# Performance work log

Measured on AMD Instinct MI355X. Metric: run time of the kernel, lower is better.

The kernel has to match this reference:

```python
import jax, jax.numpy as jnp
import numpy as np

N, E = 100000, 800000
H, C = 4, 32
HC = H * C


def setup_inputs() -> dict:
    key = jax.random.key(0)
    ks = jax.random.split(key, 32)

    def lin(k, fi, fo):
        return jax.random.normal(k, (fi, fo), jnp.float32) / np.sqrt(fi)

    inp = {
        "x": jax.random.normal(ks[0], (N, 2), jnp.float32),
        "edge_index": jax.random.randint(ks[1], (2, E), 0, N, jnp.int64),
        "edge_attr": jax.random.normal(ks[2], (E, 1), jnp.float32),
        # layer 0 (in=2)
        "Wq0": lin(ks[3], 2, HC), "bq0": jnp.zeros((HC,), jnp.float32),
        "Wk0": lin(ks[4], 2, HC), "bk0": jnp.zeros((HC,), jnp.float32),
        "Wv0": lin(ks[5], 2, HC), "bv0": jnp.zeros((HC,), jnp.float32),
        "We0": lin(ks[6], 1, HC),
        "Ws0": lin(ks[7], 2, HC), "bs0": jnp.zeros((HC,), jnp.float32),
        # layer 1 (in=HC)
        "Wq1": lin(ks[8], HC, HC), "bq1": jnp.zeros((HC,), jnp.float32),
        "Wk1": lin(ks[9], HC, HC), "bk1": jnp.zeros((HC,), jnp.float32),
        "Wv1": lin(ks[10], HC, HC), "bv1": jnp.zeros((HC,), jnp.float32),
        "We1": lin(ks[11], 1, HC),
        "Ws1": lin(ks[12], HC, HC), "bs1": jnp.zeros((HC,), jnp.float32),
        # classifier
        "Wc1": lin(ks[13], HC, 128), "bc1": jnp.zeros((128,), jnp.float32),
        "Wc2": lin(ks[14], 128, 64), "bc2": jnp.zeros((64,), jnp.float32),
        "Wc3": lin(ks[15], 64, 1), "bc3": jnp.zeros((1,), jnp.float32),
    }
    return inp


def _tconv(x, src, dst, edge_attr, Wq, bq, Wk, bk, Wv, bv, We, Ws, bs):
    # PyG TransformerConv (concat=True, root_weight=True, beta=False)
    n = x.shape[0]
    q = (x @ Wq + bq).reshape(n, H, C)
    k = (x @ Wk + bk).reshape(n, H, C)
    v = (x @ Wv + bv).reshape(n, H, C)
    e = (edge_attr @ We).reshape(-1, H, C)            # [E,H,C]
    k_j = k[src] + e
    v_j = v[src] + e
    alpha = jnp.einsum("ehc,ehc->eh", q[dst], k_j) / np.sqrt(C)  # [E,H]
    m = jax.ops.segment_max(alpha, dst, num_segments=n)          # [n,H]
    m = jnp.where(jnp.isfinite(m), m, 0.0)            # nodes with no in-edges
    ex = jnp.exp(alpha - m[dst])
    denom = jax.ops.segment_sum(ex, dst, num_segments=n)
    w = ex / (denom[dst] + 1e-16)                      # per-edge softmax weight
    out = jax.ops.segment_sum(v_j * w[:, :, None], dst, num_segments=n)
    return out.reshape(n, HC) + x @ Ws + bs


def reference(x, edge_index, edge_attr,
              Wq0, bq0, Wk0, bk0, Wv0, bv0, We0, Ws0, bs0,
              Wq1, bq1, Wk1, bk1, Wv1, bv1, We1, Ws1, bs1,
              Wc1, bc1, Wc2, bc2, Wc3, bc3):
    src, dst = edge_index[0], edge_index[1]
    h = jax.nn.relu(_tconv(x, src, dst, edge_attr, Wq0, bq0, Wk0, bk0, Wv0, bv0, We0, Ws0, bs0))
    h = jax.nn.relu(_tconv(h, src, dst, edge_attr, Wq1, bq1, Wk1, bk1, Wv1, bv1, We1, Ws1, bs1))
    # classifier (dropout inactive in eval)
    h = jax.nn.relu(h @ Wc1 + bc1)
    h = jax.nn.relu(h @ Wc2 + bc2)
    return h @ Wc3 + bc3
```

## Files before the change

### kernel.cpp

```cpp
#include <hip/hip_runtime.h>
#include <hip/hip_bf16.h>
#include <cstdio>
#include <cstdint>


typedef short s16x8 __attribute__((ext_vector_type(8)));
typedef float f32x4 __attribute__((ext_vector_type(4)));

static inline int cdiv(int a, int b) { return (a + b - 1) / b; }

#define EXP2F(x) __builtin_amdgcn_exp2f(x)
#define LOG2E 1.4426950408889634f
#define RSC 0.17677669529663687f

__device__ __forceinline__ float bflo(unsigned u) {
    union { unsigned i; float f; } x; x.i = u << 16; return x.f;
}
__device__ __forceinline__ float bfhi(unsigned u) {
    union { unsigned i; float f; } x; x.i = u & 0xffff0000u; return x.f;
}
__device__ __forceinline__ unsigned short f2b(float f) {
    __hip_bfloat16 h = __float2bfloat16(f);
    return *reinterpret_cast<unsigned short*>(&h);
}
__device__ __forceinline__ unsigned packbf(float lo, float hi) {
    return (unsigned)f2b(lo) | ((unsigned)f2b(hi) << 16);
}


__global__ __launch_bounds__(256) void hist_kernel(const int* __restrict__ dst, int E,
                                                   int* __restrict__ counts) {
    int e = blockIdx.x * 256 + threadIdx.x;
    if (e < E) atomicAdd(&counts[dst[e]], 1);
}

__global__ __launch_bounds__(256) void scan_sums(const int* __restrict__ counts, int n,
                                                 int* __restrict__ bsums) {
    __shared__ int red[256];
    int base = blockIdx.x * 2048 + threadIdx.x * 8;
    int s = 0;
#pragma unroll
    for (int j = 0; j < 8; ++j) {
        int i = base + j;
        if (i < n) s += counts[i];
    }
    red[threadIdx.x] = s;
    __syncthreads();
    for (int off = 128; off > 0; off >>= 1) {
        if (threadIdx.x < off) red[threadIdx.x] += red[threadIdx.x + off];
        __syncthreads();
    }
    if (threadIdx.x == 0) bsums[blockIdx.x] = red[0];
}

__global__ void scan_mid(int* bsums, int nb, int* offsets, int n) {
    if (blockIdx.x == 0 && threadIdx.x == 0) {
        int run = 0;
        for (int i = 0; i < nb; ++i) { int t = bsums[i]; bsums[i] = run; run += t; }
        offsets[n] = run;
    }
}

__global__ __launch_bounds__(256) void scan_out(const int* __restrict__ counts, int n,
                                                const int* __restrict__ bsums,
                                                int* __restrict__ offsets) {
    __shared__ int tsum[256];
    int base = blockIdx.x * 2048 + threadIdx.x * 8;
    int v[8];
    int s = 0;
#pragma unroll
    for (int j = 0; j < 8; ++j) {
        int i = base + j;
        v[j] = (i < n) ? counts[i] : 0;
        s += v[j];
    }
    tsum[threadIdx.x] = s;
    __syncthreads();
    for (int off = 1; off < 256; off <<= 1) {
        int x = (threadIdx.x >= (unsigned)off) ? tsum[threadIdx.x - off] : 0;
        __syncthreads();
        tsum[threadIdx.x] += x;
        __syncthreads();
    }
    int excl = tsum[threadIdx.x] - s + bsums[blockIdx.x];
#pragma unroll
    for (int j = 0; j < 8; ++j) {
        int i = base + j;
        if (i < n) { offsets[i] = excl; excl += v[j]; }
    }
}

__global__ __launch_bounds__(256) void scatter_kernel(const int* __restrict__ src,
                                                      const int* __restrict__ dst,
                                                      const float* __restrict__ ea, int E,
                                                      const int* __restrict__ offsets,
                                                      int* __restrict__ counts,
                                                      int* __restrict__ csr_off,
                                                      float* __restrict__ csr_ea) {
    int e = blockIdx.x * 256 + threadIdx.x;
    if (e >= E) return;
    int d = dst[e];
    int r = atomicSub(&counts[d], 1);
    int p = offsets[d] + r - 1;
    csr_off[p] = src[e] << 9;
    csr_ea[p] = ea[e];
}


__global__ __launch_bounds__(256) void pack_w_kernel(
    const float* __restrict__ Wq1, const float* __restrict__ Wk1,
    const float* __restrict__ Wv1, const float* __restrict__ Ws1,
    const float* __restrict__ Wc1, const float* __restrict__ Wc2,
    unsigned short* __restrict__ wpk,
    const float* __restrict__ Wq0, const float* __restrict__ bq0,
    const float* __restrict__ Wk0, const float* __restrict__ bk0,
    const float* __restrict__ We0, float* __restrict__ gcoef) {
    if (blockIdx.x == 352) {
        int t = threadIdx.x;
        if (t < 48) {
            int h = t / 12, r = t % 12, i = r >> 2, j = r & 3;
            const float* A = (i == 0) ? Wq0 : (i == 1) ? (Wq0 + 128) : bq0;
            const float* B = (j == 0) ? Wk0 : (j == 1) ? (Wk0 + 128) : (j == 2) ? We0 : bk0;
            float s = 0.f;
            for (int c = 0; c < 32; ++c) s += A[h * 32 + c] * B[h * 32 + c];
            gcoef[h * 12 + i * 4 + j] = s * (RSC * LOG2E);
        }
        return;
    }
    int idx = blockIdx.x * 256 + threadIdx.x;
    int local, COLS;
    const float* W;
    if (idx < 81920) {
        int m = idx >> 14;
        local = idx & 16383;
        COLS = 128;
        W = (m == 0) ? Wq1 : (m == 1) ? Wk1 : (m == 2) ? Wv1 : (m == 3) ? Ws1 : Wc1;
    } else {
        local = idx - 81920;
        COLS = 64;
        W = Wc2;
    }
    int CT = COLS >> 4;
    int j = local & 7, lane = (local >> 3) & 63, t = local >> 9;
    int ct = t % CT, kc = t / CT;
    int k = kc * 32 + ((lane >> 4) << 3) + j;
    int nn = (ct << 4) + (lane & 15);
    wpk[idx] = f2b(W[k * COLS + nn]);
}


__global__ __launch_bounds__(256) void agg0_kernel(
    const float* __restrict__ x, const float* __restrict__ gcoef,
    float4* __restrict__ agg4,
    const int* __restrict__ offsets, const int* __restrict__ csr_off,
    const float* __restrict__ csr_ea, int n_nodes) {
    int tid = blockIdx.x * 256 + threadIdx.x;
    int n = tid >> 2, h = tid & 3;
    if (n >= n_nodes) return;
    float2 xn = ((const float2*)x)[n];
    const float4* G4 = (const float4*)gcoef;
    float4 g0 = G4[h * 3 + 0], g1 = G4[h * 3 + 1], g2 = G4[h * 3 + 2];
    float c0 = fmaf(xn.y, g1.x, fmaf(xn.x, g0.x, g2.x));
    float c1 = fmaf(xn.y, g1.y, fmaf(xn.x, g0.y, g2.y));
    float c2 = fmaf(xn.y, g1.z, fmaf(xn.x, g0.z, g2.z));
    float c3 = fmaf(xn.y, g1.w, fmaf(xn.x, g0.w, g2.w));
    int beg = offsets[n], end = offsets[n + 1];
    float d = 0.f, X0 = 0.f, X1 = 0.f, EA = 0.f;
    for (int j = beg; j < end; ++j) {
        int off = csr_off[j];
        float e = csr_ea[j];
        float2 xs = *(const float2*)((const char*)x + (off >> 6));
        float al = fmaf(c0, xs.x, fmaf(c1, xs.y, fmaf(c2, e, c3)));
        float w = EXP2F(fminf(al, 72.f));
        d += w;
        X0 = fmaf(w, xs.x, X0);
        X1 = fmaf(w, xs.y, X1);
        EA = fmaf(w, e, EA);
    }
    agg4[(size_t)n * 4 + h] = make_float4(X0, X1, EA, d);
}


__global__ __launch_bounds__(256) void expand0_kernel(
    const float* __restrict__ x, const float4* __restrict__ agg4,
    const float* __restrict__ Wv, const float* __restrict__ bv,
    const float* __restrict__ We, const float* __restrict__ Ws,
    const float* __restrict__ bs, uint2* __restrict__ H0, int n_nodes) {
    int gid = blockIdx.x * 256 + threadIdx.x;
    int n = gid >> 5, g = gid & 31;
    if (n >= n_nodes) return;
    int h = g >> 3;
    float4 ag = agg4[(size_t)n * 4 + h];
    float inv = 1.f / (ag.w + 1e-16f);
    float2 xn = ((const float2*)x)[n];
    float4 wv0 = ((const float4*)Wv)[g], wv1 = ((const float4*)(Wv + 128))[g];
    float4 we = ((const float4*)We)[g], bv4 = ((const float4*)bv)[g];
    float4 ws0 = ((const float4*)Ws)[g], ws1 = ((const float4*)(Ws + 128))[g];
    float4 bs4 = ((const float4*)bs)[g];
    float o0 = fmaf(wv0.x, ag.x, fmaf(wv1.x, ag.y, fmaf(we.x, ag.z, bv4.x * ag.w))) * inv
             + fmaf(xn.x, ws0.x, fmaf(xn.y, ws1.x, bs4.x));
    float o1 = fmaf(wv0.y, ag.x, fmaf(wv1.y, ag.y, fmaf(we.y, ag.z, bv4.y * ag.w))) * inv
             + fmaf(xn.x, ws0.y, fmaf(xn.y, ws1.y, bs4.y));
    float o2 = fmaf(wv0.z, ag.x, fmaf(wv1.z, ag.y, fmaf(we.z, ag.z, bv4.z * ag.w))) * inv
             + fmaf(xn.x, ws0.z, fmaf(xn.y, ws1.z, bs4.z));
    float o3 = fmaf(wv0.w, ag.x, fmaf(wv1.w, ag.y, fmaf(we.w, ag.z, bv4.w * ag.w))) * inv
             + fmaf(xn.x, ws0.w, fmaf(xn.y, ws1.w, bs4.w));
    uint2 o;
    o.x = packbf(fmaxf(o0, 0.f), fmaxf(o1, 0.f));
    o.y = packbf(fmaxf(o2, 0.f), fmaxf(o3, 0.f));
    H0[(size_t)n * 32 + g] = o;
}


__global__ __launch_bounds__(64) void agg1_kernel(
    const uint2* __restrict__ Q2, const unsigned short* __restrict__ KV,
    const float* __restrict__ We, const uint2* __restrict__ S2,
    uint2* __restrict__ Hout, const int* __restrict__ offsets,
    const int* __restrict__ csr_off, const float* __restrict__ csr_ea,
    int n_nodes) {
    int lane = threadIdx.x & 63;
    int h = lane & 31, half = lane >> 5;
    int n = blockIdx.x;
    if (n >= n_nodes) return;
    size_t rb = (size_t)n * 32;
    const float sc = RSC * LOG2E;
    uint2 qp = Q2[rb + h];
    float q0 = bflo(qp.x) * sc, q1 = bfhi(qp.x) * sc;
    float q2 = bflo(qp.y) * sc, q3 = bfhi(qp.y) * sc;
    float4 we4 = ((const float4*)We)[h];
    float qwe = fmaf(q3, we4.w, fmaf(q2, we4.z, fmaf(q1, we4.y, q0 * we4.x)));
    qwe += __shfl_xor(qwe, 1);
    qwe += __shfl_xor(qwe, 2);
    qwe += __shfl_xor(qwe, 4);
    int beg = __builtin_amdgcn_readfirstlane(offsets[n]);
    int end = __builtin_amdgcn_readfirstlane(offsets[n + 1]);
    float dA = 0.f, a0A = 0.f, a1A = 0.f, a2A = 0.f, a3A = 0.f, eA = 0.f;
    float dB = 0.f, a0B = 0.f, a1B = 0.f, a2B = 0.f, a3B = 0.f, eB = 0.f;
    int lane_b = h << 3;
    for (int j = beg + half; j < end; j += 4) {
        int jB = j + 2;
        bool vB = jB < end;
        int jmB = vB ? jB : j;
        int offA = csr_off[j], offB = csr_off[jmB];
        float eaA = csr_ea[j], eaB = csr_ea[jmB];
        const char* kvA = (const char*)KV + (size_t)(unsigned)offA + lane_b;
        const char* kvB = (const char*)KV + (size_t)(unsigned)offB + lane_b;
        uint2 kA = *(const uint2*)kvA;
        uint2 vA = *(const uint2*)(kvA + 256);
        uint2 kB = *(const uint2*)kvB;
        uint2 vB2 = *(const uint2*)(kvB + 256);
        {
            float p = fmaf(q3, bfhi(kA.y), fmaf(q2, bflo(kA.y),
                      fmaf(q1, bfhi(kA.x), q0 * bflo(kA.x))));
            p += __shfl_xor(p, 1);
            p += __shfl_xor(p, 2);
            p += __shfl_xor(p, 4);
            float al = fminf(fmaf(eaA, qwe, p), 72.f);
            float w = EXP2F(al);
            dA += w;
            a0A = fmaf(w, bflo(vA.x), a0A);
            a1A = fmaf(w, bfhi(vA.x), a1A);
            a2A = fmaf(w, bflo(vA.y), a2A);
            a3A = fmaf(w, bfhi(vA.y), a3A);
            eA = fmaf(w, eaA, eA);
        }
        {
            float p = fmaf(q3, bfhi(kB.y), fmaf(q2, bflo(kB.y),
                      fmaf(q1, bfhi(kB.x), q0 * bflo(kB.x))));
            p += __shfl_xor(p, 1);
            p += __shfl_xor(p, 2);
            p += __shfl_xor(p, 4);
            float al = fmaf(eaB, qwe, p);
            al = vB ? al : -3.0e38f;
            float w = EXP2F(fminf(al, 72.f));
            dB += w;
            a0B = fmaf(w, bflo(vB2.x), a0B);
            a1B = fmaf(w, bfhi(vB2.x), a1B);
            a2B = fmaf(w, bflo(vB2.y), a2B);
            a3B = fmaf(w, bfhi(vB2.y), a3B);
            eB = fmaf(w, eaB, eB);
        }
    }
    float d = dA + dB;
    float a0 = a0A + a0B, a1 = a1A + a1B, a2 = a2A + a2B, a3 = a3A + a3B;
    float ea = eA + eB;
    d += __shfl_xor(d, 32);
    a0 += __shfl_xor(a0, 32);
    a1 += __shfl_xor(a1, 32);
    a2 += __shfl_xor(a2, 32);
    a3 += __shfl_xor(a3, 32);
    ea += __shfl_xor(ea, 32);
    if (half == 0) {
        float inv = 1.f / (d + 1e-16f);
        uint2 sp = S2[rb + h];
        uint2 o;
        o.x = packbf(fmaxf(fmaf(a0 + we4.x * ea, inv, bflo(sp.x)), 0.f),
                     fmaxf(fmaf(a1 + we4.y * ea, inv, bfhi(sp.x)), 0.f));
        o.y = packbf(fmaxf(fmaf(a2 + we4.z * ea, inv, bflo(sp.y)), 0.f),
                     fmaxf(fmaf(a3 + we4.w * ea, inv, bfhi(sp.y)), 0.f));
        Hout[rb + h] = o;
    }
}


__global__ __launch_bounds__(256) void gemm4_kernel(
    const unsigned short* __restrict__ Hb, int n_nodes,
    const unsigned short* __restrict__ wpk,
    const float* __restrict__ B0, unsigned short* __restrict__ O0, int ld0,
    const float* __restrict__ B1, unsigned short* __restrict__ O1, int ld1,
    const float* __restrict__ B2, unsigned short* __restrict__ O2, int ld2,
    const float* __restrict__ B3, unsigned short* __restrict__ O3, int ld3) {
    int wid = threadIdx.x >> 6, lane = threadIdx.x & 63;
    int lr = lane & 15, lk = lane >> 4;
    int rbase = blockIdx.x * 128 + wid * 32;
    s16x8 b[2][4];
#pragma unroll
    for (int nt = 0; nt < 2; ++nt) {
        int row = min(rbase + nt * 16 + lr, n_nodes - 1);
        const s16x8* hp = (const s16x8*)(Hb + (size_t)row * 128);
#pragma unroll
        for (int kc = 0; kc < 4; ++kc) b[nt][kc] = hp[kc * 4 + lk];
    }
    const float* Bm[4] = {B0, B1, B2, B3};
    unsigned short* Om[4] = {O0, O1, O2, O3};
    int ldm[4] = {ld0, ld1, ld2, ld3};
#pragma unroll
    for (int mm = 0; mm < 4; ++mm) {
        const s16x8* wp = (const s16x8*)(wpk + mm * 16384);
        f32x4 acc[2][8];
#pragma unroll
        for (int nt = 0; nt < 2; ++nt)
#pragma unroll
            for (int ct = 0; ct < 8; ++ct) acc[nt][ct] = (f32x4){0.f, 0.f, 0.f, 0.f};
#pragma unroll
        for (int kc = 0; kc < 4; ++kc) {
#pragma unroll
            for (int ct = 0; ct < 8; ++ct) {
                s16x8 a = wp[(kc * 8 + ct) * 64 + lane];
                acc[0][ct] = __builtin_amdgcn_mfma_f32_16x16x32_bf16(a, b[0][kc], acc[0][ct], 0, 0, 0);
                acc[1][ct] = __builtin_amdgcn_mfma_f32_16x16x32_bf16(a, b[1][kc], acc[1][ct], 0, 0, 0);
            }
        }
        const float* Bp = Bm[mm];
        unsigned short* Op = Om[mm];
        int ld = ldm[mm];
#pragma unroll
        for (int ct = 0; ct < 8; ++ct) {
            float4 bb = *(const float4*)(Bp + ct * 16 + lk * 4);
#pragma unroll
            for (int nt = 0; nt < 2; ++nt) {
                int node = rbase + nt * 16 + lr;
                if (node < n_nodes) {
                    uint2 o;
                    o.x = packbf(acc[nt][ct][0] + bb.x, acc[nt][ct][1] + bb.y);
                    o.y = packbf(acc[nt][ct][2] + bb.z, acc[nt][ct][3] + bb.w);
                    ((uint2*)(Op + (size_t)node * ld))[ct * 4 + lk] = o;
                }
            }
        }
    }
}


__global__ __launch_bounds__(256) void classifier_kernel(
    const unsigned short* __restrict__ H1b, int n_nodes,
    const unsigned short* __restrict__ wc1p, const float* __restrict__ bc1,
    const unsigned short* __restrict__ wc2p, const float* __restrict__ bc2,
    const float* __restrict__ Wc3, const float* __restrict__ bc3,
    float* __restrict__ out) {
    __shared__ char lds_raw[4 * 16 * 272];
    int wid = threadIdx.x >> 6, lane = threadIdx.x & 63;
    int lr = lane & 15, lk = lane >> 4;
    int nb = blockIdx.x * 64 + wid * 16;
    char* tile = lds_raw + wid * 16 * 272;

    s16x8 b[4];
    {
        int row = min(nb + lr, n_nodes - 1);
        const s16x8* hp = (const s16x8*)(H1b + (size_t)row * 128);
#pragma unroll
        for (int kc = 0; kc < 4; ++kc) b[kc] = hp[kc * 4 + lk];
    }
    f32x4 acc[8];
#pragma unroll
    for (int ct = 0; ct < 8; ++ct) acc[ct] = (f32x4){0.f, 0.f, 0.f, 0.f};
#pragma unroll
    for (int kc = 0; kc < 4; ++kc)
#pragma unroll
        for (int ct = 0; ct < 8; ++ct) {
            s16x8 a = ((const s16x8*)wc1p)[(kc * 8 + ct) * 64 + lane];
            acc[ct] = __builtin_amdgcn_mfma_f32_16x16x32_bf16(a, b[kc], acc[ct], 0, 0, 0);
        }
#pragma unroll
    for (int ct = 0; ct < 8; ++ct) {
        float4 bb = *(const float4*)(bc1 + ct * 16 + lk * 4);
        uint2 o;
        o.x = packbf(fmaxf(acc[ct][0] + bb.x, 0.f), fmaxf(acc[ct][1] + bb.y, 0.f));
        o.y = packbf(fmaxf(acc[ct][2] + bb.z, 0.f), fmaxf(acc[ct][3] + bb.w, 0.f));
        *(uint2*)(tile + lr * 272 + ct * 32 + lk * 8) = o;
    }
    __syncthreads();
    s16x8 b2[4];
#pragma unroll
    for (int kc = 0; kc < 4; ++kc)
        b2[kc] = *(const s16x8*)(tile + lr * 272 + kc * 64 + lk * 16);
    f32x4 acc2[4];
#pragma unroll
    for (int ct = 0; ct < 4; ++ct) acc2[ct] = (f32x4){0.f, 0.f, 0.f, 0.f};
#pragma unroll
    for (int kc = 0; kc < 4; ++kc)
#pragma unroll
        for (int ct = 0; ct < 4; ++ct) {
            s16x8 a = ((const s16x8*)wc2p)[(kc * 4 + ct) * 64 + lane];
            acc2[ct] = __builtin_amdgcn_mfma_f32_16x16x32_bf16(a, b2[kc], acc2[ct], 0, 0, 0);
        }
    float part = 0.f;
#pragma unroll
    for (int ct = 0; ct < 4; ++ct) {
        int ch0 = ct * 16 + lk * 4;
        float4 bb = *(const float4*)(bc2 + ch0);
        float4 w3 = *(const float4*)(Wc3 + ch0);
        part += fmaxf(acc2[ct][0] + bb.x, 0.f) * w3.x;
        part += fmaxf(acc2[ct][1] + bb.y, 0.f) * w3.y;
        part += fmaxf(acc2[ct][2] + bb.z, 0.f) * w3.z;
        part += fmaxf(acc2[ct][3] + bb.w, 0.f) * w3.w;
    }
    part += __shfl_xor(part, 16);
    part += __shfl_xor(part, 32);
    if (lk == 0) {
        int node = nb + lr;
        if (node < n_nodes) out[node] = part + bc3[0];
    }
}


extern "C" void kernel_launch(void* const* d_in, const int* in_sizes, int n_in,
                              void* d_out, int out_size, void* d_ws, size_t ws_size,
                              hipStream_t stream) {
    const float* x = (const float*)d_in[0];
    const int* ei = (const int*)d_in[1];
    const float* ea = (const float*)d_in[2];
    const float *Wq0 = (const float*)d_in[3], *bq0 = (const float*)d_in[4];
    const float *Wk0 = (const float*)d_in[5], *bk0 = (const float*)d_in[6];
    const float *Wv0 = (const float*)d_in[7], *bv0 = (const float*)d_in[8];
    const float* We0 = (const float*)d_in[9];
    const float *Ws0 = (const float*)d_in[10], *bs0 = (const float*)d_in[11];
    const float *Wq1 = (const float*)d_in[12], *bq1 = (const float*)d_in[13];
    const float *Wk1 = (const float*)d_in[14], *bk1 = (const float*)d_in[15];
    const float *Wv1 = (const float*)d_in[16], *bv1 = (const float*)d_in[17];
    const float* We1 = (const float*)d_in[18];
    const float *Ws1 = (const float*)d_in[19], *bs1 = (const float*)d_in[20];
    const float *Wc1 = (const float*)d_in[21], *bc1 = (const float*)d_in[22];
    const float *Wc2 = (const float*)d_in[23], *bc2 = (const float*)d_in[24];
    const float *Wc3 = (const float*)d_in[25], *bc3 = (const float*)d_in[26];

    const int N = in_sizes[0] / 2;
    const int E = in_sizes[2];
    const int* src = ei;
    const int* dst = ei + E;

    size_t NM = (size_t)N * 128;
    float4* agg4 = (float4*)d_ws;
    float* gcoef = (float*)(agg4 + (size_t)N * 4);
    unsigned short* H0b = (unsigned short*)(gcoef + 64);
    unsigned short* Qb = H0b + NM;
    unsigned short* KV = Qb + NM;
    unsigned short* S1b = KV + 2 * NM;
    unsigned short* wpk = S1b + NM;
    int* counts = (int*)(wpk + 90112);
    int* offsets = counts + N;
    int* bsums = offsets + N + 1;
    int* csr_off = bsums + 256;
    float* csr_ea = (float*)(csr_off + E);
    size_t need = (size_t)((char*)(csr_ea + E) - (char*)d_ws);
    if (need > ws_size) {
        fprintf(stderr, "kernel_launch: ws too small (need %zu, have %zu)\n", need, ws_size);
        return;
    }

    const int NB_SCAN = cdiv(N, 2048);

    hipMemsetAsync(counts, 0, (size_t)N * 4, stream);
    hist_kernel<<<cdiv(E, 256), 256, 0, stream>>>(dst, E, counts);
    scan_sums<<<NB_SCAN, 256, 0, stream>>>(counts, N, bsums);
    scan_mid<<<1, 64, 0, stream>>>(bsums, NB_SCAN, offsets, N);
    scan_out<<<NB_SCAN, 256, 0, stream>>>(counts, N, bsums, offsets);
    scatter_kernel<<<cdiv(E, 256), 256, 0, stream>>>(src, dst, ea, E, offsets, counts,
                                                     csr_off, csr_ea);
    pack_w_kernel<<<353, 256, 0, stream>>>(Wq1, Wk1, Wv1, Ws1, Wc1, Wc2, wpk,
                                           Wq0, bq0, Wk0, bk0, We0, gcoef);

    agg0_kernel<<<cdiv(N * 4, 256), 256, 0, stream>>>(
        x, gcoef, agg4, offsets, csr_off, csr_ea, N);
    expand0_kernel<<<cdiv(N * 32, 256), 256, 0, stream>>>(
        x, agg4, Wv0, bv0, We0, Ws0, bs0, (uint2*)H0b, N);

    gemm4_kernel<<<cdiv(N, 128), 256, 0, stream>>>(
        H0b, N, wpk,
        bq1, Qb, 128,
        bk1, KV, 256,
        bv1, KV + 128, 256,
        bs1, S1b, 128);
    agg1_kernel<<<N, 64, 0, stream>>>(
        (const uint2*)Qb, KV, We1, (const uint2*)S1b, (uint2*)S1b,
        offsets, csr_off, csr_ea, N);

    classifier_kernel<<<cdiv(N, 64), 256, 0, stream>>>(
        S1b, N, wpk + 65536, bc1, wpk + 81920, bc2, Wc3, bc3, (float*)d_out);
}
```

Baseline: 385.3 us.

## Stage gemm4 weights in LDS and coalesce output stores through LDS tile

The gemm4 kernel now copies each 32KB weight matrix into shared memory once per block instead of having every wave read it from global/L2. Outputs are written to an LDS tile first and then stored as full 16-byte rows, replacing scattered 8-byte stores. It also sets launch bounds to 2 blocks per CU. The cost is about 67KB of LDS per block, extra barriers, and weight reloads that are serialized with compute rather than overlapped.

```diff
diff --git a/kernel.cpp b/kernel.cpp
--- a/kernel.cpp
+++ b/kernel.cpp
@@ -303,20 +303,24 @@
 }
 
 
-__global__ __launch_bounds__(256) void gemm4_kernel(
+__global__ __launch_bounds__(256, 2) void gemm4_kernel(
     const unsigned short* __restrict__ Hb, int n_nodes,
     const unsigned short* __restrict__ wpk,
     const float* __restrict__ B0, unsigned short* __restrict__ O0, int ld0,
     const float* __restrict__ B1, unsigned short* __restrict__ O1, int ld1,
     const float* __restrict__ B2, unsigned short* __restrict__ O2, int ld2,
     const float* __restrict__ B3, unsigned short* __restrict__ O3, int ld3) {
-    int wid = threadIdx.x >> 6, lane = threadIdx.x & 63;
+    __shared__ unsigned short wbuf[16384];
+    __shared__ char tbuf[128 * 272];
+    int tid = threadIdx.x;
+    int wid = tid >> 6, lane = tid & 63;
     int lr = lane & 15, lk = lane >> 4;
-    int rbase = blockIdx.x * 128 + wid * 32;
+    int nblk = blockIdx.x * 128;
+
     s16x8 b[2][4];
 #pragma unroll
     for (int nt = 0; nt < 2; ++nt) {
-        int row = min(rbase + nt * 16 + lr, n_nodes - 1);
+        int row = min(nblk + wid * 32 + nt * 16 + lr, n_nodes - 1);
         const s16x8* hp = (const s16x8*)(Hb + (size_t)row * 128);
 #pragma unroll
         for (int kc = 0; kc < 4; ++kc) b[nt][kc] = hp[kc * 4 + lk];
@@ -324,9 +328,15 @@
     const float* Bm[4] = {B0, B1, B2, B3};
     unsigned short* Om[4] = {O0, O1, O2, O3};
     int ldm[4] = {ld0, ld1, ld2, ld3};
+
+#pragma unroll
+    for (int i = 0; i < 8; ++i) {
+        int c = i * 256 + tid;
+        ((uint4*)wbuf)[c] = ((const uint4*)wpk)[c];
+    }
 #pragma unroll
     for (int mm = 0; mm < 4; ++mm) {
-        const s16x8* wp = (const s16x8*)(wpk + mm * 16384);
+        __syncthreads();
         f32x4 acc[2][8];
 #pragma unroll
         for (int nt = 0; nt < 2; ++nt)
@@ -336,26 +346,41 @@
         for (int kc = 0; kc < 4; ++kc) {
 #pragma unroll
             for (int ct = 0; ct < 8; ++ct) {
-                s16x8 a = wp[(kc * 8 + ct) * 64 + lane];
+                s16x8 a = ((const s16x8*)wbuf)[(kc * 8 + ct) * 64 + lane];
                 acc[0][ct] = __builtin_amdgcn_mfma_f32_16x16x32_bf16(a, b[0][kc], acc[0][ct], 0, 0, 0);
                 acc[1][ct] = __builtin_amdgcn_mfma_f32_16x16x32_bf16(a, b[1][kc], acc[1][ct], 0, 0, 0);
             }
         }
         const float* Bp = Bm[mm];
+#pragma unroll
+        for (int ct = 0; ct < 8; ++ct) {
+            float4 bb = *(const float4*)(Bp + ct * 16 + lk * 4);
+#pragma unroll
+            for (int nt = 0; nt < 2; ++nt) {
+                int rnode = wid * 32 + nt * 16 + lr;
+                uint2 o;
+                o.x = packbf(acc[nt][ct][0] + bb.x, acc[nt][ct][1] + bb.y);
+                o.y = packbf(acc[nt][ct][2] + bb.z, acc[nt][ct][3] + bb.w);
+                *(uint2*)(tbuf + rnode * 272 + ct * 32 + lk * 8) = o;
+            }
+        }
+        __syncthreads();
         unsigned short* Op = Om[mm];
         int ld = ldm[mm];
 #pragma unroll
-        for (int ct = 0; ct < 8; ++ct) {
-            float4 bb = *(const float4*)(Bp + ct * 16 + lk * 4);
-#pragma unroll
-            for (int nt = 0; nt < 2; ++nt) {
-                int node = rbase + nt * 16 + lr;
-                if (node < n_nodes) {
-                    uint2 o;
-                    o.x = packbf(acc[nt][ct][0] + bb.x, acc[nt][ct][1] + bb.y);
-                    o.y = packbf(acc[nt][ct][2] + bb.z, acc[nt][ct][3] + bb.w);
-                    ((uint2*)(Op + (size_t)node * ld))[ct * 4 + lk] = o;
-                }
+        for (int i = 0; i < 8; ++i) {
+            int chunk = i * 256 + tid;
+            int nd = chunk >> 4, c16 = chunk & 15;
+            int ng = nblk + nd;
+            uint4 v = *(const uint4*)(tbuf + nd * 272 + c16 * 16);
+            if (ng < n_nodes) *(uint4*)(Op + (size_t)ng * ld + c16 * 8) = v;
+        }
+        if (mm < 3) {
+            const uint4* ws = (const uint4*)(wpk + (mm + 1) * 16384);
+#pragma unroll
+            for (int i = 0; i < 8; ++i) {
+                int c = i * 256 + tid;
+                ((uint4*)wbuf)[c] = ws[c];
             }
         }
     }
```

Measured after the change: 353.1 us. -8.4%, faster.
